# Kernel optimization log

Measured on AMD Instinct MI355X. Metric: run time of the kernel, lower is better.

Reference implementation:

```python
import jax, jax.numpy as jnp
import numpy as np

RATIOS = [0.9, 0.7, 0.5, 0.3]
EPS = 1e-5


def _layernorm(x, g, b):
    m = jnp.mean(x, axis=-1, keepdims=True)
    v = jnp.mean(jnp.square(x - m), axis=-1, keepdims=True)
    return (x - m) * jax.lax.rsqrt(v + EPS) * g + b


def _stage(x, g, b, W, bias):
    return _layernorm(x, g, b) @ W + bias


def _prune(x, W1, b1, W2, b2, ratio):
    B, N, C = x.shape
    stats = jnp.mean(x, axis=1)                       # (B, C)
    scores = jax.nn.relu(stats @ W1 + b1) @ W2 + b2    # (B, C)
    k = max(1, int(C * ratio))
    _, idx = jax.lax.top_k(jax.lax.stop_gradient(scores), k)  # (B, k)
    hard = jnp.zeros((B, C), scores.dtype).at[jnp.arange(B)[:, None], idx].set(1.0)
    soft = jax.nn.sigmoid(scores)
    # straight-through: forward value == hard, gradient flows through soft
    mask = hard + soft - jax.lax.stop_gradient(soft)
    return x * mask[:, None, :]


def setup_inputs() -> dict:
    key = jax.random.key(0)
    dims = [(96, 96), (96, 192), (192, 384), (384, 768)]
    inp = {}
    ks = jax.random.split(key, 64)
    ki = iter(ks)
    inp["x"] = jax.random.normal(next(ki), (32, 3136, 96), dtype=jnp.float32)
    for i, (din, dout) in enumerate(dims, 1):
        inp[f"s{i}_g"] = jnp.ones((din,), jnp.float32)
        inp[f"s{i}_b"] = jnp.zeros((din,), jnp.float32)
        inp[f"s{i}_W"] = jax.random.normal(next(ki), (din, dout), jnp.float32) * 0.02
        inp[f"s{i}_bias"] = jnp.zeros((dout,), jnp.float32)
        d = dout
        inp[f"p{i}_W1"] = jax.random.normal(next(ki), (d, d // 4), jnp.float32) * 0.02
        inp[f"p{i}_b1"] = jnp.zeros((d // 4,), jnp.float32)
        inp[f"p{i}_W2"] = jax.random.normal(next(ki), (d // 4, d), jnp.float32) * 0.02
        inp[f"p{i}_b2"] = jnp.zeros((d,), jnp.float32)
    inp["H"] = 56
    inp["W"] = 56
    return inp


def reference(x,
              s1_g, s1_b, s1_W, s1_bias, p1_W1, p1_b1, p1_W2, p1_b2,
              s2_g, s2_b, s2_W, s2_bias, p2_W1, p2_b1, p2_W2, p2_b2,
              s3_g, s3_b, s3_W, s3_bias, p3_W1, p3_b1, p3_W2, p3_b2,
              s4_g, s4_b, s4_W, s4_bias, p4_W1, p4_b1, p4_W2, p4_b2,
              H, W):
    x = _stage(x, s1_g, s1_b, s1_W, s1_bias)
    x = _prune(x, p1_W1, p1_b1, p1_W2, p1_b2, RATIOS[0])
    x = _stage(x, s2_g, s2_b, s2_W, s2_bias)
    x = _prune(x, p2_W1, p2_b1, p2_W2, p2_b2, RATIOS[1])
    x = _stage(x, s3_g, s3_b, s3_W, s3_bias)
    x = _prune(x, p3_W1, p3_b1, p3_W2, p3_b2, RATIOS[2])
    x = _stage(x, s4_g, s4_b, s4_W, s4_bias)
    x = _prune(x, p4_W1, p4_b1, p4_W2, p4_b2, RATIOS[3])
    return x
```

## Files before the change

kernel.cpp:

```cpp
#include <hip/hip_runtime.h>
#include <hip/hip_bf16.h>
#include <stdint.h>

#define NTOK 3136
#define MTOT 100352
#define RPW  14
#define WPB  224

typedef __attribute__((ext_vector_type(8))) short bf16x8;
typedef __attribute__((ext_vector_type(4))) float f32x4;
typedef __attribute__((ext_vector_type(2))) float f32x2;

static __device__ __forceinline__ ushort f2bf(float x) {
  union { float f; uint32_t u; } c; c.f = x;
  uint32_t r = (c.u + 0x7FFFu + ((c.u >> 16) & 1u)) >> 16;
  return (ushort)r;
}
static __device__ __forceinline__ float bf2f(ushort h) {
  union { uint32_t u; float f; } c; c.u = ((uint32_t)h) << 16;
  return c.f;
}

template<int DIN, bool WLO>
__global__ __launch_bounds__(256)
void ln_colsum_k(const float* __restrict__ in, const float* __restrict__ gma,
                 const float* __restrict__ bta, ushort* __restrict__ oh,
                 ushort* __restrict__ ol, float* __restrict__ part)
{
  constexpr int P2 = DIN / 2;
  constexpr int T2 = (P2 + 63) / 64;
  const int wid  = (blockIdx.x * 256 + threadIdx.x) >> 6;
  const int lane = threadIdx.x & 63;
  const int b = wid / WPB;
  const int w = wid - b * WPB;

  f32x2 gv[T2], bv[T2], acc[T2];
#pragma unroll
  for (int t = 0; t < T2; ++t) {
    int c2 = lane + 64 * t;
    if (c2 < P2) {
      gv[t] = *(const f32x2*)(gma + 2 * c2);
      bv[t] = *(const f32x2*)(bta + 2 * c2);
    } else { gv[t] = {0.f, 0.f}; bv[t] = {0.f, 0.f}; }
    acc[t] = {0.f, 0.f};
  }

  const size_t rbase = ((size_t)b * NTOK + (size_t)w * RPW) * DIN;
  const float* ip = in + rbase;
  ushort* oph = oh + rbase;
  ushort* opl = ol + rbase;

  for (int j = 0; j < RPW; ++j) {
    f32x2 v[T2];
    float s = 0.f, sq = 0.f;
#pragma unroll
    for (int t = 0; t < T2; ++t) {
      int c2 = lane + 64 * t;
      f32x2 xv = {0.f, 0.f};
      if (c2 < P2) xv = *(const f32x2*)(ip + (size_t)j * DIN + 2 * c2);
      v[t] = xv;
      s  += xv[0] + xv[1];
      sq += xv[0] * xv[0] + xv[1] * xv[1];
    }
#pragma unroll
    for (int off = 1; off < 64; off <<= 1) {
      s  += __shfl_xor(s, off);
      sq += __shfl_xor(sq, off);
    }
    float m   = s / (float)DIN;
    float var = sq / (float)DIN - m * m;
    float r   = 1.f / sqrtf(var + 1e-5f);
#pragma unroll
    for (int t = 0; t < T2; ++t) {
      int c2 = lane + 64 * t;
      if (c2 < P2) {
        float xn0 = (v[t][0] - m) * r * gv[t][0] + bv[t][0];
        float xn1 = (v[t][1] - m) * r * gv[t][1] + bv[t][1];
        ushort h0 = f2bf(xn0), h1 = f2bf(xn1);
        ((uint32_t*)(oph + (size_t)j * DIN))[c2] =
            (uint32_t)h0 | ((uint32_t)h1 << 16);
        if (WLO) {
          ushort l0 = f2bf(xn0 - bf2f(h0)), l1 = f2bf(xn1 - bf2f(h1));
          ((uint32_t*)(opl + (size_t)j * DIN))[c2] =
              (uint32_t)l0 | ((uint32_t)l1 << 16);
        }
        acc[t][0] += xn0;
        acc[t][1] += xn1;
      }
    }
  }
#pragma unroll
  for (int t = 0; t < T2; ++t) {
    int c2 = lane + 64 * t;
    if (c2 < P2) {
      int c = 2 * c2;
      part[((size_t)b * DIN + c) * WPB + w]     = acc[t][0];
      part[((size_t)b * DIN + c + 1) * WPB + w] = acc[t][1];
    }
  }
}

template<int DIN, int DOUT, int SLOTS, bool CMP, int CMPN, int RLEN, bool GLO>
__global__ __launch_bounds__(1024)
void scores_k(const float* __restrict__ part,
              const float* __restrict__ Wt, const float* __restrict__ bias,
              const float* __restrict__ W1, const float* __restrict__ b1,
              const float* __restrict__ W2, const float* __restrict__ b2,
              float* __restrict__ mask, int k,
              const ushort* __restrict__ whi, const ushort* __restrict__ wlo,
              ushort* __restrict__ wch, ushort* __restrict__ wcl,
              int* __restrict__ list_g, float* __restrict__ biasc)
{
  constexpr int DH  = DOUT / 4;
  constexpr int DH4 = DH / 4;
  constexpr int NSLC = (1024 / DH4 < 64) ? 1024 / DH4 : 64;
  constexpr int RPSC = (DOUT + NSLC - 1) / NSLC;
  constexpr int C4  = DOUT / 4;
  constexpr int NSLD = (1024 / C4 < 64) ? 1024 / C4 : 64;
  constexpr int RPSD = (DH + NSLD - 1) / NSLD;

  __shared__ float xm[DIN];
  __shared__ float st[DOUT];
  __shared__ float h[DH];
  __shared__ float sc[DOUT];
  __shared__ float red[4096];
  __shared__ int lsh[256];

  const int b = blockIdx.x, tid = threadIdx.x;

  if constexpr (SLOTS == 25) {
    if (tid < DIN) {
      const float* p = part + ((size_t)b * DIN + tid) * 25;
      float s = 0.f;
#pragma unroll
      for (int i = 0; i < 25; ++i) s += p[i];
      xm[tid] = s * (1.f / (float)NTOK);
    }
  } else {
    const int cg = tid >> 2, wq = tid & 3;
    if (cg < DIN) {
      const float* p = part + ((size_t)b * DIN + cg) * WPB + wq * 56;
      f32x4 a = {0.f, 0.f, 0.f, 0.f};
#pragma unroll
      for (int u = 0; u < 14; ++u) {
        f32x4 t0 = *(const f32x4*)(p + u * 4);
        a[0] += t0[0]; a[1] += t0[1]; a[2] += t0[2]; a[3] += t0[3];
      }
      red[wq * DIN + cg] = (a[0] + a[1]) + (a[2] + a[3]);
    }
    __syncthreads();
    if (tid < DIN)
      xm[tid] = ((red[0 * DIN + tid] + red[1 * DIN + tid]) +
                 (red[2 * DIN + tid] + red[3 * DIN + tid])) * (1.f / (float)NTOK);
  }
  __syncthreads();

  {
    constexpr int RPS = DIN / 4;
    const int j4 = tid % C4, sl = tid / C4;
    if (sl < 4) {
      const float* wp = Wt + (size_t)(sl * RPS) * DOUT + j4 * 4;
      f32x4 acc = {0.f, 0.f, 0.f, 0.f};
#pragma unroll
      for (int r = 0; r < RPS; ++r) {
        f32x4 wv = *(const f32x4*)(wp + (size_t)r * DOUT);
        float xv = xm[sl * RPS + r];
        acc[0] = fmaf(xv, wv[0], acc[0]);
        acc[1] = fmaf(xv, wv[1], acc[1]);
        acc[2] = fmaf(xv, wv[2], acc[2]);
        acc[3] = fmaf(xv, wv[3], acc[3]);
      }
      *(f32x4*)&red[sl * DOUT + j4 * 4] = acc;
    }
  }
  __syncthreads();
  if (tid < DOUT)
    st[tid] = ((red[0 * DOUT + tid] + red[1 * DOUT + tid]) +
               (red[2 * DOUT + tid] + red[3 * DOUT + tid])) + bias[tid];
  __syncthreads();

  {
    const int j4 = tid % DH4, sl = tid / DH4;
    if (sl < NSLC) {
      f32x4 acc = {0.f, 0.f, 0.f, 0.f};
#pragma unroll
      for (int rr = 0; rr < RPSC; ++rr) {
        int r = sl * RPSC + rr;
        if (r < DOUT) {
          f32x4 wv = *(const f32x4*)(W1 + (size_t)r * DH + j4 * 4);
          float sv = st[r];
          acc[0] = fmaf(sv, wv[0], acc[0]);
          acc[1] = fmaf(sv, wv[1], acc[1]);
          acc[2] = fmaf(sv, wv[2], acc[2]);
          acc[3] = fmaf(sv, wv[3], acc[3]);
        }
      }
      *(f32x4*)&red[(size_t)sl * DH + j4 * 4] = acc;
    }
  }
  __syncthreads();
  if (tid < DH) {
    float a = 0.f;
#pragma unroll 4
    for (int sl = 0; sl < NSLC; ++sl) a += red[(size_t)sl * DH + tid];
    h[tid] = fmaxf(b1[tid] + a, 0.f);
  }
  __syncthreads();

  {
    const int c4 = tid % C4, sl = tid / C4;
    if (sl < NSLD) {
      f32x4 acc = {0.f, 0.f, 0.f, 0.f};
#pragma unroll
      for (int rr = 0; rr < RPSD; ++rr) {
        int r = sl * RPSD + rr;
        if (r < DH) {
          f32x4 wv = *(const f32x4*)(W2 + (size_t)r * DOUT + c4 * 4);
          float hv = h[r];
          acc[0] = fmaf(hv, wv[0], acc[0]);
          acc[1] = fmaf(hv, wv[1], acc[1]);
          acc[2] = fmaf(hv, wv[2], acc[2]);
          acc[3] = fmaf(hv, wv[3], acc[3]);
        }
      }
      *(f32x4*)&red[(size_t)sl * DOUT + c4 * 4] = acc;
    }
  }
  __syncthreads();
  for (int c = tid; c < DOUT; c += 1024) {
    float a = 0.f;
#pragma unroll 4
    for (int sl = 0; sl < NSLD; ++sl) a += red[(size_t)sl * DOUT + c];
    sc[c] = b2[c] + a;
  }
  __syncthreads();

  for (int c = tid; c < DOUT; c += 1024) {
    float v = sc[c];
    int rank = 0;
#pragma unroll 8
    for (int j = 0; j < DOUT; ++j) {
      float u = sc[j];
      rank += (u > v) || (u == v && j < c);
    }
    mask[(size_t)b * DOUT + c] = (rank < k) ? 1.f : 0.f;
    if (CMP && rank < k) lsh[rank] = c;
  }
  if constexpr (CMP) {
    if (tid >= k && tid < CMPN) lsh[tid] = -1;
    __syncthreads();
    if (tid < CMPN) {
      int c = lsh[tid];
      list_g[b * 256 + tid] = c;
      biasc[b * 256 + tid] = (c >= 0) ? bias[c] : 0.f;
    }
    constexpr int U4 = RLEN / 8;
    for (int idx = tid; idx < CMPN * U4; idx += 1024) {
      int j = idx / U4, u = idx - j * U4;
      int src = lsh[j];
      uint4 v = make_uint4(0u, 0u, 0u, 0u);
      if (src >= 0) v = *(const uint4*)(whi + (size_t)src * RLEN + u * 8);
      *(uint4*)(wch + ((size_t)b * CMPN + j) * RLEN + u * 8) = v;
      if constexpr (GLO) {
        uint4 vl = make_uint4(0u, 0u, 0u, 0u);
        if (src >= 0) vl = *(const uint4*)(wlo + (size_t)src * RLEN + u * 8);
        *(uint4*)(wcl + ((size_t)b * CMPN + j) * RLEN + u * 8) = vl;
      }
    }
  }
}

__global__ __launch_bounds__(256)
void convW_all_k(const float* __restrict__ W0, const float* __restrict__ W1,
                 const float* __restrict__ W2, const float* __restrict__ W3,
                 ushort* __restrict__ hi, ushort* __restrict__ lo)
{
  const int Kd[4]   = { 96, 96, 192, 384 };
  const int Nd[4]   = { 96, 192, 384, 768 };
  const int off[5]  = { 0, 12288, 36864, 110592, 405504 };
  const float* Wp[4] = { W0, W1, W2, W3 };

  int idx = blockIdx.x * 256 + threadIdx.x;
  if (idx >= 405504) return;
  int s = (idx >= off[1]) + (idx >= off[2]) + (idx >= off[3]);
  int local = idx - off[s];
  int K = Kd[s], N = Nd[s];
  int n = local / K, kk = local - n * K;
  float v = (n < N) ? Wp[s][(size_t)kk * N + n] : 0.f;
  ushort h = f2bf(v);
  hi[idx] = h;
  lo[idx] = f2bf(v - bf2f(h));
}

#define ASYNC16(GP, LP) __builtin_amdgcn_global_load_lds( \
    (const __attribute__((address_space(1))) void*)(GP),  \
    (__attribute__((address_space(3))) void*)(LP), 16, 0, 0)

template<int K, int NSEG, int BNL, int N, int NWN, bool WLO>
__global__ __launch_bounds__(128 * NWN)
void gemm_ln_k(const ushort* __restrict__ a0, const ushort* __restrict__ a1,
               const ushort* __restrict__ a2,
               const ushort* __restrict__ b0, const ushort* __restrict__ b1,
               const ushort* __restrict__ b2,
               const float* __restrict__ bias, const float* __restrict__ msk,
               const float* __restrict__ gnext, const float* __restrict__ bnext,
               ushort* __restrict__ oh, ushort* __restrict__ ol,
               float* __restrict__ part)
{
  constexpr int T   = 128 * NWN;
  constexpr int R   = T / 4;
  constexpr int AI  = 128 / R;
  constexpr int BI  = BNL / R;
  constexpr int IS  = AI + BI;
  constexpr int WN  = N / NWN;
  constexpr int NFR = WN / 16;
  constexpr int KSTEPS = K / 32;
  constexpr int NT  = NSEG * KSTEPS;
  __shared__ __align__(16) ushort ldsA[3][128 * 32];
  __shared__ __align__(16) ushort ldsB[3][BNL * 32];

  const int tid  = threadIdx.x;
  const int lane = tid & 63;
  const int wid  = tid >> 6;
  const int wm = wid & 1, wn = wid >> 1;

  const int q8  = gridDim.x >> 3;
  const int bid = blockIdx.x;
  const int mt  = (bid & 7) * q8 + (bid >> 3);
  const size_t row0 = (size_t)mt * 128;

  const ushort* Aseg[3] = { a0, a1, a2 };
  const ushort* Bseg[3] = { b0, b1, b2 };

  f32x4 acc[4][NFR];
#pragma unroll
  for (int i = 0; i < 4; ++i)
#pragma unroll
    for (int j = 0; j < NFR; ++j) acc[i][j] = { 0.f, 0.f, 0.f, 0.f };

  const int c_row  = tid >> 2;
  const int c_phys = tid & 3;

#define STAGEF(BUF, TT)                                                        \
  {                                                                            \
    const int seg_ = (TT) / KSTEPS;                                            \
    const int k0_  = ((TT) % KSTEPS) * 32;                                     \
    const ushort* ap_ = Aseg[seg_];                                            \
    const ushort* bp_ = Bseg[seg_];                                            \
    _Pragma("unroll")                                                          \
    for (int r_ = 0; r_ < AI; ++r_) {                                          \
      int row_  = c_row + r_ * R;                                              \
      int slot_ = c_phys ^ ((row_ >> 1) & 3);                                  \
      ASYNC16(ap_ + (row0 + row_) * (size_t)K + (k0_ + slot_ * 8),             \
              &ldsA[BUF][(row_ * 4 + c_phys) * 8]);                            \
    }                                                                          \
    _Pragma("unroll")                                                          \
    for (int r_ = 0; r_ < BI; ++r_) {                                          \
      int row_  = c_row + r_ * R;                                              \
      int slot_ = c_phys ^ ((row_ >> 1) & 3);                                  \
      ASYNC16(bp_ + (size_t)row_ * K + (k0_ + slot_ * 8),                      \
              &ldsB[BUF][(row_ * 4 + c_phys) * 8]);                            \
    }                                                                          \
  }

  STAGEF(0, 0);
  STAGEF(1, 1);
#pragma unroll
  for (int t = 0; t < NT; ++t) {
    if (t == NT - 1)            { asm volatile("s_waitcnt vmcnt(0)" ::: "memory"); }
    else if constexpr (IS == 4) { asm volatile("s_waitcnt vmcnt(4)" ::: "memory"); }
    else                        { asm volatile("s_waitcnt vmcnt(5)" ::: "memory"); }
    __builtin_amdgcn_s_barrier();
    if (t + 2 < NT) STAGEF((t + 2) % 3, t + 2);
    const int buf = t % 3;
    const int slot = lane >> 4;
    const int r16  = lane & 15;
    bf16x8 af[4], bfr[NFR];
#pragma unroll
    for (int mi = 0; mi < 4; ++mi) {
      int r = wm * 64 + mi * 16 + r16;
      af[mi] = *(const bf16x8*)&ldsA[buf][(r * 4 + (slot ^ ((r >> 1) & 3))) * 8];
    }
#pragma unroll
    for (int ni = 0; ni < NFR; ++ni) {
      int r = wn * WN + ni * 16 + r16;
      bfr[ni] = *(const bf16x8*)&ldsB[buf][(r * 4 + (slot ^ ((r >> 1) & 3))) * 8];
    }
#pragma unroll
    for (int mi = 0; mi < 4; ++mi)
#pragma unroll
      for (int ni = 0; ni < NFR; ++ni)
        acc[mi][ni] = __builtin_amdgcn_mfma_f32_16x16x32_bf16(af[mi], bfr[ni],
                                                              acc[mi][ni], 0, 0, 0);
  }
#undef STAGEF

  __syncthreads();

  float* rowred = (float*)&ldsA[0][0];
  ushort* xsh = (ushort*)&ldsB[0][0];
  ushort* xsl = xsh + 32 * N;
  float* colred = (float*)(xsh + 32 * N * (WLO ? 2 : 1));

  const int l15 = lane & 15, l4 = lane >> 4;
  const int b0i = (int)(row0 / NTOK);
  const size_t rowB = (size_t)(b0i + 1) * NTOK;
  const bool strad = rowB < row0 + 128;

  float biasv[NFR], mk0a[NFR], mk1a[NFR], gvn[NFR], bvn[NFR];
#pragma unroll
  for (int ni = 0; ni < NFR; ++ni) {
    int n = wn * WN + ni * 16 + l15;
    biasv[ni] = bias[n];
    mk0a[ni] = msk[(size_t)b0i * N + n];
    mk1a[ni] = strad ? msk[(size_t)(b0i + 1) * N + n] : mk0a[ni];
    gvn[ni] = gnext[n];
    bvn[ni] = bnext[n];
  }

  float rs[16], rq[16];
#pragma unroll
  for (int i = 0; i < 16; ++i) { rs[i] = 0.f; rq[i] = 0.f; }
#pragma unroll
  for (int mi = 0; mi < 4; ++mi)
#pragma unroll
    for (int q = 0; q < 4; ++q) {
      size_t row = row0 + wm * 64 + mi * 16 + l4 * 4 + q;
      bool loB = row < rowB;
#pragma unroll
      for (int ni = 0; ni < NFR; ++ni) {
        float v = (acc[mi][ni][q] + biasv[ni]) * (loB ? mk0a[ni] : mk1a[ni]);
        acc[mi][ni][q] = v;
        rs[mi * 4 + q] += v;
        rq[mi * 4 + q] += v * v;
      }
    }
#pragma unroll
  for (int off = 1; off < 16; off <<= 1)
#pragma unroll
    for (int i = 0; i < 16; ++i) {
      rs[i] += __shfl_xor(rs[i], off);
      rq[i] += __shfl_xor(rq[i], off);
    }
  if (l15 == 0) {
#pragma unroll
    for (int mi = 0; mi < 4; ++mi)
#pragma unroll
      for (int q = 0; q < 4; ++q) {
        int r = wm * 64 + mi * 16 + l4 * 4 + q;
        rowred[(wn * 128 + r) * 2 + 0] = rs[mi * 4 + q];
        rowred[(wn * 128 + r) * 2 + 1] = rq[mi * 4 + q];
      }
  }
  __syncthreads();

  float mean[16], rstd[16];
#pragma unroll
  for (int mi = 0; mi < 4; ++mi)
#pragma unroll
    for (int q = 0; q < 4; ++q) {
      int r = wm * 64 + mi * 16 + l4 * 4 + q;
      float S = 0.f, Q = 0.f;
#pragma unroll
      for (int w = 0; w < NWN; ++w) {
        S += rowred[(w * 128 + r) * 2 + 0];
        Q += rowred[(w * 128 + r) * 2 + 1];
      }
      float mn  = S / (float)N;
      float var = Q / (float)N - mn * mn;
      mean[mi * 4 + q] = mn;
      rstd[mi * 4 + q] = 1.f / sqrtf(var + 1e-5f);
    }

  float cs0[NFR], cs1[NFR];
#pragma unroll
  for (int ni = 0; ni < NFR; ++ni) { cs0[ni] = 0.f; cs1[ni] = 0.f; }
#pragma unroll
  for (int mi = 0; mi < 4; ++mi) {
    __syncthreads();
#pragma unroll
    for (int q = 0; q < 4; ++q) {
      const int rl = l4 * 4 + q;
      const size_t row = row0 + wm * 64 + mi * 16 + rl;
      const bool loB = row < rowB;
      const float mn = mean[mi * 4 + q], rv = rstd[mi * 4 + q];
#pragma unroll
      for (int ni = 0; ni < NFR; ++ni) {
        const int n = wn * WN + ni * 16 + l15;
        float xn = (acc[mi][ni][q] - mn) * rv * gvn[ni] + bvn[ni];
        ushort hh = f2bf(xn);
        xsh[(wm * 16 + rl) * N + n] = hh;
        if constexpr (WLO) xsl[(wm * 16 + rl) * N + n] = f2bf(xn - bf2f(hh));
        if (loB) cs0[ni] += xn; else cs1[ni] += xn;
      }
    }
    __syncthreads();
    constexpr int U4R = N / 8;
    for (int idx = tid; idx < 32 * U4R; idx += T) {
      const int grp = idx / U4R, c = idx - grp * U4R;
      const size_t row = row0 + (grp >> 4) * 64 + mi * 16 + (grp & 15);
      *(uint4*)(oh + row * (size_t)N + c * 8) =
          *(const uint4*)(xsh + grp * N + c * 8);
      if constexpr (WLO)
        *(uint4*)(ol + row * (size_t)N + c * 8) =
            *(const uint4*)(xsl + grp * N + c * 8);
    }
  }

#pragma unroll
  for (int ni = 0; ni < NFR; ++ni) {
    cs0[ni] += __shfl_xor(cs0[ni], 16);
    cs0[ni] += __shfl_xor(cs0[ni], 32);
    cs1[ni] += __shfl_xor(cs1[ni], 16);
    cs1[ni] += __shfl_xor(cs1[ni], 32);
  }
  __syncthreads();
  if (l4 == 0) {
#pragma unroll
    for (int ni = 0; ni < NFR; ++ni) {
      int n = wn * WN + ni * 16 + l15;
      colred[(0 * 2 + wm) * N + n] = cs0[ni];
      colred[(1 * 2 + wm) * N + n] = cs1[ni];
    }
  }
  __syncthreads();
  if (wm == 0 && l4 == 0) {
    const int mt_lo = (b0i * NTOK) >> 7;
    const int slot0 = mt - mt_lo;
#pragma unroll
    for (int ni = 0; ni < NFR; ++ni) {
      int n = wn * WN + ni * 16 + l15;
      float t0 = colred[0 * N + n] + colred[1 * N + n];
      part[((size_t)b0i * N + n) * 25 + slot0] = t0;
      if (strad) {
        float t1 = colred[2 * N + n] + colred[3 * N + n];
        part[((size_t)(b0i + 1) * N + n) * 25 + 0] = t1;
      }
    }
  }
}

template<int K, int NC, int N>
__global__ __launch_bounds__(256)
void gemm_lnc_k(const ushort* __restrict__ ahi, const ushort* __restrict__ alo,
                const ushort* __restrict__ wch, const ushort* __restrict__ wcl,
                const int* __restrict__ list, const float* __restrict__ biasc,
                const float* __restrict__ gnext, const float* __restrict__ bnext,
                ushort* __restrict__ oh, float* __restrict__ part)
{
  constexpr int KSTEPS = K / 32;
  constexpr int NT  = 3 * KSTEPS;
  constexpr int WN  = NC / 2;
  constexpr int NFR = WN / 16;
  __shared__ __align__(16) ushort ldsA[3][128 * 32];
  __shared__ __align__(16) ushort ldsB[3][NC * 32];
  __shared__ float rowred[2][128][2];
  __shared__ float rowmnrv[128];
  __shared__ float rowrv[128];

  const int tid  = threadIdx.x;
  const int lane = tid & 63;
  const int wid  = tid >> 6;
  const int wm = wid & 1, wn = wid >> 1;

  const int q8  = gridDim.x >> 3;
  const int bid = blockIdx.x;
  const int wg  = (bid & 7) * q8 + (bid >> 3);
  const int b   = wg / 25;
  const int mt  = wg - b * 25;
  const size_t row0 = (size_t)b * NTOK + (size_t)mt * 128;
  const size_t rowEnd = (size_t)(b + 1) * NTOK;
  const int rows_valid = (mt == 24) ? 64 : 128;

  const ushort* Aseg[3] = { ahi, ahi, alo };
  const ushort* Bseg[3] = { wch + (size_t)b * NC * K, wcl + (size_t)b * NC * K,
                            wch + (size_t)b * NC * K };

  f32x4 acc[4][NFR];
#pragma unroll
  for (int i = 0; i < 4; ++i)
#pragma unroll
    for (int j = 0; j < NFR; ++j) acc[i][j] = { 0.f, 0.f, 0.f, 0.f };

  const int c_row  = tid >> 2;
  const int c_phys = tid & 3;

#define STAGEL(BUF, TT)                                                        \
  {                                                                            \
    const int seg_ = (TT) / KSTEPS;                                            \
    const int k0_  = ((TT) % KSTEPS) * 32;                                     \
    const ushort* ap_ = Aseg[seg_];                                            \
    const ushort* bp_ = Bseg[seg_];                                            \
    _Pragma("unroll")                                                          \
    for (int r_ = 0; r_ < 2; ++r_) {                                           \
      int row_  = c_row + r_ * 64;                                             \
      int slot_ = c_phys ^ ((row_ >> 1) & 3);                                  \
      size_t ar_ = row0 + row_;                                                \
      if (ar_ >= rowEnd) ar_ = rowEnd - 1;                                     \
      ASYNC16(ap_ + ar_ * (size_t)K + (k0_ + slot_ * 8),                       \
              &ldsA[BUF][(row_ * 4 + c_phys) * 8]);                            \
    }                                                                          \
    _Pragma("unroll")                                                          \
    for (int r_ = 0; r_ < 3; ++r_) {                                           \
      int row_  = c_row + r_ * 64;                                             \
      int slot_ = c_phys ^ ((row_ >> 1) & 3);                                  \
      ASYNC16(bp_ + (size_t)row_ * K + (k0_ + slot_ * 8),                      \
              &ldsB[BUF][(row_ * 4 + c_phys) * 8]);                            \
    }                                                                          \
  }

  STAGEL(0, 0);
  STAGEL(1, 1);
#pragma unroll
  for (int t = 0; t < NT; ++t) {
    if (t == NT - 1) { asm volatile("s_waitcnt vmcnt(0)" ::: "memory"); }
    else             { asm volatile("s_waitcnt vmcnt(5)" ::: "memory"); }
    __builtin_amdgcn_s_barrier();
    if (t + 2 < NT) STAGEL((t + 2) % 3, t + 2);
    const int buf = t % 3;
    const int slot = lane >> 4;
    const int r16  = lane & 15;
    bf16x8 af[4], bfr[NFR];
#pragma unroll
    for (int mi = 0; mi < 4; ++mi) {
      int r = wm * 64 + mi * 16 + r16;
      af[mi] = *(const bf16x8*)&ldsA[buf][(r * 4 + (slot ^ ((r >> 1) & 3))) * 8];
    }
#pragma unroll
    for (int ni = 0; ni < NFR; ++ni) {
      int r = wn * WN + ni * 16 + r16;
      bfr[ni] = *(const bf16x8*)&ldsB[buf][(r * 4 + (slot ^ ((r >> 1) & 3))) * 8];
    }
#pragma unroll
    for (int mi = 0; mi < 4; ++mi)
#pragma unroll
      for (int ni = 0; ni < NFR; ++ni)
        acc[mi][ni] = __builtin_amdgcn_mfma_f32_16x16x32_bf16(af[mi], bfr[ni],
                                                              acc[mi][ni], 0, 0, 0);
  }
#undef STAGEL

  __syncthreads();

  const int l15 = lane & 15, l4 = lane >> 4;

  int   nj[NFR];
  float biasv[NFR];
#pragma unroll
  for (int ni = 0; ni < NFR; ++ni) {
    int j = wn * WN + ni * 16 + l15;
    nj[ni]    = list[b * 256 + j];
    biasv[ni] = biasc[b * 256 + j];
  }

  float rs[16], rq[16];
#pragma unroll
  for (int i = 0; i < 16; ++i) { rs[i] = 0.f; rq[i] = 0.f; }
#pragma unroll
  for (int mi = 0; mi < 4; ++mi)
#pragma unroll
    for (int q = 0; q < 4; ++q) {
#pragma unroll
      for (int ni = 0; ni < NFR; ++ni) {
        float v = acc[mi][ni][q] + biasv[ni];
        acc[mi][ni][q] = v;
        rs[mi * 4 + q] += v;
        rq[mi * 4 + q] += v * v;
      }
    }
#pragma unroll
  for (int off = 1; off < 16; off <<= 1)
#pragma unroll
    for (int i = 0; i < 16; ++i) {
      rs[i] += __shfl_xor(rs[i], off);
      rq[i] += __shfl_xor(rq[i], off);
    }
  if (l15 == 0) {
#pragma unroll
    for (int mi = 0; mi < 4; ++mi)
#pragma unroll
      for (int q = 0; q < 4; ++q) {
        int r = wm * 64 + mi * 16 + l4 * 4 + q;
        rowred[wn][r][0] = rs[mi * 4 + q];
        rowred[wn][r][1] = rq[mi * 4 + q];
      }
  }
  __syncthreads();
  if (tid < 128) {
    float S = rowred[0][tid][0] + rowred[1][tid][0];
    float Q = rowred[0][tid][1] + rowred[1][tid][1];
    float mn = S / (float)N;
    float rv = 1.f / sqrtf(Q / (float)N - mn * mn + 1e-5f);
    rowmnrv[tid] = mn * rv;
    rowrv[tid]   = rv;
  }
  __syncthreads();

  float* sbuf = (float*)&ldsB[0][0];
  float colS = 0.f, colS2 = 0.f;

#pragma unroll
  for (int h = 0; h < 8; ++h) {
    if (h * 16 >= rows_valid) break;
    __syncthreads();
    for (int idx = tid; idx < 16 * N / 4; idx += 256)
      ((f32x4*)sbuf)[idx] = f32x4{0.f, 0.f, 0.f, 0.f};
    __syncthreads();
    if ((h >> 2) == wm) {
      const int mi = h & 3;
#pragma unroll
      for (int q = 0; q < 4; ++q) {
        const int rl = l4 * 4 + q;
        const float rv = rowrv[h * 16 + rl];
#pragma unroll
        for (int ni = 0; ni < NFR; ++ni)
          sbuf[rl * N + nj[ni]] = acc[mi][ni][q] * rv;
      }
    }
    __syncthreads();
    {
      float a = 0.f;
#pragma unroll
      for (int rl = 0; rl < 16; ++rl) a += sbuf[rl * N + tid];
      colS += a;
      if (tid < N - 256) {
        float a2 = 0.f;
        const int c2 = 256 + tid;
#pragma unroll
        for (int rl = 0; rl < 16; ++rl) a2 += sbuf[rl * N + c2];
        colS2 += a2;
      }
    }
    for (int idx = tid; idx < 16 * (N / 8); idx += 256) {
      const int rl = idx / (N / 8), cg = idx - rl * (N / 8);
      const float mnrv = rowmnrv[h * 16 + rl];
      const float* sp = sbuf + rl * N + cg * 8;
      f32x4 s0 = *(const f32x4*)(sp);
      f32x4 s1 = *(const f32x4*)(sp + 4);
      f32x4 g0 = *(const f32x4*)(gnext + cg * 8);
      f32x4 g1 = *(const f32x4*)(gnext + cg * 8 + 4);
      f32x4 e0 = *(const f32x4*)(bnext + cg * 8);
      f32x4 e1 = *(const f32x4*)(bnext + cg * 8 + 4);
      uint32_t w[4];
#pragma unroll
      for (int j = 0; j < 2; ++j) {
        ushort ha = f2bf(g0[2*j]   * (s0[2*j]   - mnrv) + e0[2*j]);
        ushort hb = f2bf(g0[2*j+1] * (s0[2*j+1] - mnrv) + e0[2*j+1]);
        w[j] = (uint32_t)ha | ((uint32_t)hb << 16);
      }
#pragma unroll
      for (int j = 0; j < 2; ++j) {
        ushort ha = f2bf(g1[2*j]   * (s1[2*j]   - mnrv) + e1[2*j]);
        ushort hb = f2bf(g1[2*j+1] * (s1[2*j+1] - mnrv) + e1[2*j+1]);
        w[2 + j] = (uint32_t)ha | ((uint32_t)hb << 16);
      }
      *(uint4*)(oh + (row0 + h * 16 + rl) * (size_t)N + cg * 8) =
          make_uint4(w[0], w[1], w[2], w[3]);
    }
  }

  float msum = 0.f;
  for (int r = 0; r < rows_valid; ++r) msum += rowmnrv[r];
  {
    const int c = tid;
    part[((size_t)b * N + c) * 25 + mt] =
        gnext[c] * (colS - msum) + (float)rows_valid * bnext[c];
    if (tid < N - 256) {
      const int c2 = 256 + tid;
      part[((size_t)b * N + c2) * 25 + mt] =
          gnext[c2] * (colS2 - msum) + (float)rows_valid * bnext[c2];
    }
  }
}

template<int K>
__global__ __launch_bounds__(512)
void gemm_c4_k(const ushort* __restrict__ A, const ushort* __restrict__ Wc,
               const int* __restrict__ list, const float* __restrict__ biasc,
               float* __restrict__ C)
{
  constexpr int NT = K / 32;
  __shared__ __align__(16) ushort ldsA[3][128 * 32];
  __shared__ __align__(16) ushort ldsB[3][256 * 32];

  const int tid  = threadIdx.x;
  const int lane = tid & 63;
  const int wid  = tid >> 6;
  const int wm = wid & 1, wn = wid >> 1;

  const int q8  = gridDim.x >> 3;
  const int bid = blockIdx.x;
  const int wg  = (bid & 7) * q8 + (bid >> 3);
  const int b   = wg / 25;
  const int mt  = wg - b * 25;
  const size_t row0 = (size_t)b * NTOK + (size_t)mt * 128;
  const int rows_valid = (mt == 24) ? 64 : 128;

  const ushort* bp = Wc + (size_t)b * 256 * K;

  const int c_row  = tid >> 2;
  const int c_phys = tid & 3;

  size_t arow = row0 + c_row;
  const size_t rowEnd = (size_t)(b + 1) * NTOK;
  if (arow >= rowEnd) arow = rowEnd - 1;
  const ushort* apr = A + arow * (size_t)K;

  f32x4 acc[4][4];
#pragma unroll
  for (int i = 0; i < 4; ++i)
#pragma unroll
    for (int j = 0; j < 4; ++j) acc[i][j] = { 0.f, 0.f, 0.f, 0.f };

#define STAGEC(BUF, TT)                                                        \
  {                                                                            \
    const int k0_ = (TT) * 32;                                                 \
    {                                                                          \
      int slot_ = c_phys ^ ((c_row >> 1) & 3);                                 \
      ASYNC16(apr + (k0_ + slot_ * 8),                                         \
              &ldsA[BUF][(c_row * 4 + c_phys) * 8]);                           \
    }                                                                          \
    _Pragma("unroll")                                                          \
    for (int r_ = 0; r_ < 2; ++r_) {                                           \
      int row_  = c_row + r_ * 128;                                            \
      int slot_ = c_phys ^ ((row_ >> 1) & 3);                                  \
      ASYNC16(bp + (size_t)row_ * K + (k0_ + slot_ * 8),                       \
              &ldsB[BUF][(row_ * 4 + c_phys) * 8]);                            \
    }                                                                          \
  }

  STAGEC(0, 0);
  STAGEC(1, 1);
#pragma unroll
  for (int t = 0; t < NT; ++t) {
    if (t == NT - 1) { asm volatile("s_waitcnt vmcnt(0)" ::: "memory"); }
    else             { asm volatile("s_waitcnt vmcnt(3)" ::: "memory"); }
    __builtin_amdgcn_s_barrier();
    if (t + 2 < NT) STAGEC((t + 2) % 3, t + 2);
    const int buf = t % 3;
    const int slot = lane >> 4;
    const int r16  = lane & 15;
    bf16x8 af[4], bfr[4];
#pragma unroll
    for (int mi = 0; mi < 4; ++mi) {
      int r = wm * 64 + mi * 16 + r16;
      af[mi] = *(const bf16x8*)&ldsA[buf][(r * 4 + (slot ^ ((r >> 1) & 3))) * 8];
    }
#pragma unroll
    for (int ni = 0; ni < 4; ++ni) {
      int r = wn * 64 + ni * 16 + r16;
      bfr[ni] = *(const bf16x8*)&ldsB[buf][(r * 4 + (slot ^ ((r >> 1) & 3))) * 8];
    }
#pragma unroll
    for (int mi = 0; mi < 4; ++mi)
#pragma unroll
      for (int ni = 0; ni < 4; ++ni)
        acc[mi][ni] = __builtin_amdgcn_mfma_f32_16x16x32_bf16(af[mi], bfr[ni],
                                                              acc[mi][ni], 0, 0, 0);
  }
#undef STAGEC

  float* cst = (float*)&ldsB[0][0];

  const int l15 = lane & 15, l4 = lane >> 4;
  int   nj[4];
  float biasv[4];
#pragma unroll
  for (int ni = 0; ni < 4; ++ni) {
    int j = wn * 64 + ni * 16 + l15;
    nj[ni]    = list[b * 256 + j];
    biasv[ni] = biasc[b * 256 + j];
  }

#pragma unroll
  for (int hh = 0; hh < 8; ++hh) {
    const int hrows = rows_valid - hh * 16;
    if (hrows <= 0) break;
    __syncthreads();
    for (int idx = tid; idx < 16 * 192; idx += 512)
      ((f32x4*)cst)[idx] = f32x4{0.f, 0.f, 0.f, 0.f};
    __syncthreads();
    if ((hh >> 2) == wm) {
      const int mi = hh & 3;
#pragma unroll
      for (int q = 0; q < 4; ++q) {
        const int rl = l4 * 4 + q;
#pragma unroll
        for (int ni = 0; ni < 4; ++ni)
          if (nj[ni] >= 0)
            cst[rl * 768 + nj[ni]] = acc[mi][ni][q] + biasv[ni];
      }
    }
    __syncthreads();
    const int nst = (hrows >= 16 ? 16 : hrows) * 192;
    for (int idx = tid; idx < nst; idx += 512) {
      const int grp = idx / 192, c = idx - grp * 192;
      const size_t row = row0 + hh * 16 + grp;
      *(f32x4*)(C + row * 768 + c * 4) = ((const f32x4*)cst)[grp * 192 + c];
    }
  }
}

extern "C" void kernel_launch(void* const* d_in, const int* in_sizes, int n_in,
                              void* d_out, int out_size, void* d_ws, size_t ws_size,
                              hipStream_t stream)
{
  (void)in_sizes; (void)n_in; (void)out_size; (void)ws_size;
  const float* x = (const float*)d_in[0];
  const float *sg[4], *sb[4], *sW[4], *sbias[4], *pW1[4], *pb1[4], *pW2[4], *pb2[4];
  for (int s = 0; s < 4; ++s) {
    int base = 1 + s * 8;
    sg[s]    = (const float*)d_in[base + 0];
    sb[s]    = (const float*)d_in[base + 1];
    sW[s]    = (const float*)d_in[base + 2];
    sbias[s] = (const float*)d_in[base + 3];
    pW1[s]   = (const float*)d_in[base + 4];
    pb1[s]   = (const float*)d_in[base + 5];
    pW2[s]   = (const float*)d_in[base + 6];
    pb2[s]   = (const float*)d_in[base + 7];
  }

  float* out = (float*)d_out;
  ushort* hiA = (ushort*)out;
  ushort* loA = (ushort*)(out + 19267584);
  ushort* loB = (ushort*)(out + 38535168);

  char* ws = (char*)d_ws;
  ushort* hiB  = (ushort*)(ws);
  float*  part = (float*) (ws + 77070336);
  float*  mk   = (float*) (ws + 79822848);
  ushort* w_hi = (ushort*)(ws + 79921152);
  ushort* w_lo = (ushort*)(ws + 80732160);
  ushort* wc   = (ushort*)(ws + 81543168);
  int*    lst  = (int*)   (ws + 87834624);
  float*  bsc  = (float*) (ws + 87867392);

  ushort* wch3 = wc;
  ushort* wcl3 = wc + 1179648;

  const int woff[4] = { 0, 12288, 36864, 110592 };

  convW_all_k<<<(405504 + 255) / 256, 256, 0, stream>>>(
      sW[0], sW[1], sW[2], sW[3], w_hi, w_lo);

  const int LNG = 32 * WPB / 4;

  ln_colsum_k<96, true><<<LNG, 256, 0, stream>>>(x, sg[0], sb[0], hiA, loA, part);
  scores_k<96, 96, 224, false, 256, 384, false><<<32, 1024, 0, stream>>>(
      part, sW[0], sbias[0], pW1[0], pb1[0], pW2[0], pb2[0], mk, 86,
      nullptr, nullptr, nullptr, nullptr, nullptr, nullptr);
  gemm_ln_k<96, 3, 128, 96, 2, true><<<784, 256, 0, stream>>>(
      hiA, hiA, loA, w_hi + woff[0], w_lo + woff[0], w_hi + woff[0],
      sbias[0], mk, sg[1], sb[1], hiB, loB, part);

  scores_k<96, 192, 25, false, 256, 384, false><<<32, 1024, 0, stream>>>(
      part, sW[1], sbias[1], pW1[1], pb1[1], pW2[1], pb2[1], mk, 134,
      nullptr, nullptr, nullptr, nullptr, nullptr, nullptr);
  gemm_ln_k<96, 3, 192, 192, 2, true><<<784, 256, 0, stream>>>(
      hiB, hiB, loB, w_hi + woff[1], w_lo + woff[1], w_hi + woff[1],
      sbias[1], mk, sg[2], sb[2], hiA, loA, part);

  scores_k<192, 384, 25, true, 192, 192, true><<<32, 1024, 0, stream>>>(
      part, sW[2], sbias[2], pW1[2], pb1[2], pW2[2], pb2[2], mk, 192,
      w_hi + woff[2], w_lo + woff[2], wch3, wcl3, lst, bsc);
  gemm_lnc_k<192, 192, 384><<<800, 256, 0, stream>>>(
      hiA, loA, wch3, wcl3, lst, bsc, sg[3], sb[3], hiB, part);

  scores_k<384, 768, 25, true, 256, 384, false><<<32, 1024, 0, stream>>>(
      part, sW[3], sbias[3], pW1[3], pb1[3], pW2[3], pb2[3], mk, 230,
      w_hi + woff[3], nullptr, wc, nullptr, lst, bsc);
  gemm_c4_k<384><<<800, 512, 0, stream>>>(hiB, wc, lst, bsc, out);
}
```

Baseline: 475.8 us.

## Load hi/lo operands together and run split-bf16 MFMAs per K-step

```diff
diff --git a/kernel.cpp b/kernel.cpp
--- a/kernel.cpp
+++ b/kernel.cpp
@@ -296,12 +296,10 @@
     (const __attribute__((address_space(1))) void*)(GP),  \
     (__attribute__((address_space(3))) void*)(LP), 16, 0, 0)
 
-template<int K, int NSEG, int BNL, int N, int NWN, bool WLO>
+template<int K, int BNL, int N, int NWN, bool WLO>
 __global__ __launch_bounds__(128 * NWN)
-void gemm_ln_k(const ushort* __restrict__ a0, const ushort* __restrict__ a1,
-               const ushort* __restrict__ a2,
-               const ushort* __restrict__ b0, const ushort* __restrict__ b1,
-               const ushort* __restrict__ b2,
+void gemm_ln_k(const ushort* __restrict__ ahi, const ushort* __restrict__ alo,
+               const ushort* __restrict__ bhi, const ushort* __restrict__ blo,
                const float* __restrict__ bias, const float* __restrict__ msk,
                const float* __restrict__ gnext, const float* __restrict__ bnext,
                ushort* __restrict__ oh, ushort* __restrict__ ol,
@@ -311,13 +309,13 @@
   constexpr int R   = T / 4;
   constexpr int AI  = 128 / R;
   constexpr int BI  = BNL / R;
-  constexpr int IS  = AI + BI;
+  constexpr int KS  = K / 32;
   constexpr int WN  = N / NWN;
   constexpr int NFR = WN / 16;
-  constexpr int KSTEPS = K / 32;
-  constexpr int NT  = NSEG * KSTEPS;
-  __shared__ __align__(16) ushort ldsA[3][128 * 32];
-  __shared__ __align__(16) ushort ldsB[3][BNL * 32];
+  __shared__ __align__(16) ushort ldsAh[2][128 * 32];
+  __shared__ __align__(16) ushort ldsAl[2][128 * 32];
+  __shared__ __align__(16) ushort ldsBh[2][BNL * 32];
+  __shared__ __align__(16) ushort ldsBl[2][BNL * 32];
 
   const int tid  = threadIdx.x;
   const int lane = tid & 63;
@@ -329,9 +327,6 @@
   const int mt  = (bid & 7) * q8 + (bid >> 3);
   const size_t row0 = (size_t)mt * 128;
 
-  const ushort* Aseg[3] = { a0, a1, a2 };
-  const ushort* Bseg[3] = { b0, b1, b2 };
-
   f32x4 acc[4][NFR];
 #pragma unroll
   for (int i = 0; i < 4; ++i)
@@ -341,66 +336,84 @@
   const int c_row  = tid >> 2;
   const int c_phys = tid & 3;
 
-#define STAGEF(BUF, TT)                                                        \
+#define STG(BUF, KK)                                                           \
   {                                                                            \
-    const int seg_ = (TT) / KSTEPS;                                            \
-    const int k0_  = ((TT) % KSTEPS) * 32;                                     \
-    const ushort* ap_ = Aseg[seg_];                                            \
-    const ushort* bp_ = Bseg[seg_];                                            \
+    const int k0_ = (KK) * 32;                                                 \
     _Pragma("unroll")                                                          \
     for (int r_ = 0; r_ < AI; ++r_) {                                          \
       int row_  = c_row + r_ * R;                                              \
       int slot_ = c_phys ^ ((row_ >> 1) & 3);                                  \
-      ASYNC16(ap_ + (row0 + row_) * (size_t)K + (k0_ + slot_ * 8),             \
-              &ldsA[BUF][(row_ * 4 + c_phys) * 8]);                            \
+      ASYNC16(ahi + (row0 + row_) * (size_t)K + (k0_ + slot_ * 8),             \
+              &ldsAh[BUF][(row_ * 4 + c_phys) * 8]);                           \
+      ASYNC16(alo + (row0 + row_) * (size_t)K + (k0_ + slot_ * 8),             \
+              &ldsAl[BUF][(row_ * 4 + c_phys) * 8]);                           \
     }                                                                          \
     _Pragma("unroll")                                                          \
     for (int r_ = 0; r_ < BI; ++r_) {                                          \
       int row_  = c_row + r_ * R;                                              \
       int slot_ = c_phys ^ ((row_ >> 1) & 3);                                  \
-      ASYNC16(bp_ + (size_t)row_ * K + (k0_ + slot_ * 8),                      \
-              &ldsB[BUF][(row_ * 4 + c_phys) * 8]);                            \
+      ASYNC16(bhi + (size_t)row_ * K + (k0_ + slot_ * 8),                      \
+              &ldsBh[BUF][(row_ * 4 + c_phys) * 8]);                           \
+      ASYNC16(blo + (size_t)row_ * K + (k0_ + slot_ * 8),                      \
+              &ldsBl[BUF][(row_ * 4 + c_phys) * 8]);                           \
     }                                                                          \
   }
 
-  STAGEF(0, 0);
-  STAGEF(1, 1);
-#pragma unroll
-  for (int t = 0; t < NT; ++t) {
-    if (t == NT - 1)            { asm volatile("s_waitcnt vmcnt(0)" ::: "memory"); }
-    else if constexpr (IS == 4) { asm volatile("s_waitcnt vmcnt(4)" ::: "memory"); }
-    else                        { asm volatile("s_waitcnt vmcnt(5)" ::: "memory"); }
-    __builtin_amdgcn_s_barrier();
-    if (t + 2 < NT) STAGEF((t + 2) % 3, t + 2);
-    const int buf = t % 3;
+  STG(0, 0);
+  asm volatile("s_waitcnt vmcnt(0)" ::: "memory");
+  __builtin_amdgcn_s_barrier();
+#pragma unroll
+  for (int t = 0; t < KS; ++t) {
+    if (t + 1 < KS) STG((t + 1) & 1, t + 1);
+    const int buf = t & 1;
     const int slot = lane >> 4;
     const int r16  = lane & 15;
-    bf16x8 af[4], bfr[NFR];
+    bf16x8 ah[4], al[4], bh[NFR], bl[NFR];
 #pragma unroll
     for (int mi = 0; mi < 4; ++mi) {
       int r = wm * 64 + mi * 16 + r16;
-      af[mi] = *(const bf16x8*)&ldsA[buf][(r * 4 + (slot ^ ((r >> 1) & 3))) * 8];
+      int off = (r * 4 + (slot ^ ((r >> 1) & 3))) * 8;
+      ah[mi] = *(const bf16x8*)&ldsAh[buf][off];
+      al[mi] = *(const bf16x8*)&ldsAl[buf][off];
     }
 #pragma unroll
     for (int ni = 0; ni < NFR; ++ni) {
       int r = wn * WN + ni * 16 + r16;
-      bfr[ni] = *(const bf16x8*)&ldsB[buf][(r * 4 + (slot ^ ((r >> 1) & 3))) * 8];
+      int off = (r * 4 + (slot ^ ((r >> 1) & 3))) * 8;
+      bh[ni] = *(const bf16x8*)&ldsBh[buf][off];
+      bl[ni] = *(const bf16x8*)&ldsBl[buf][off];
     }
 #pragma unroll
     for (int mi = 0; mi < 4; ++mi)
 #pragma unroll
       for (int ni = 0; ni < NFR; ++ni)
-        acc[mi][ni] = __builtin_amdgcn_mfma_f32_16x16x32_bf16(af[mi], bfr[ni],
+        acc[mi][ni] = __builtin_amdgcn_mfma_f32_16x16x32_bf16(ah[mi], bh[ni],
                                                               acc[mi][ni], 0, 0, 0);
-  }
-#undef STAGEF
-
-  __syncthreads();
-
-  float* rowred = (float*)&ldsA[0][0];
-  ushort* xsh = (ushort*)&ldsB[0][0];
-  ushort* xsl = xsh + 32 * N;
-  float* colred = (float*)(xsh + 32 * N * (WLO ? 2 : 1));
+#pragma unroll
+    for (int mi = 0; mi < 4; ++mi)
+#pragma unroll
+      for (int ni = 0; ni < NFR; ++ni)
+        acc[mi][ni] = __builtin_amdgcn_mfma_f32_16x16x32_bf16(ah[mi], bl[ni],
+                                                              acc[mi][ni], 0, 0, 0);
+#pragma unroll
+    for (int mi = 0; mi < 4; ++mi)
+#pragma unroll
+      for (int ni = 0; ni < NFR; ++ni)
+        acc[mi][ni] = __builtin_amdgcn_mfma_f32_16x16x32_bf16(al[mi], bh[ni],
+                                                              acc[mi][ni], 0, 0, 0);
+    if (t + 1 < KS) {
+      asm volatile("s_waitcnt vmcnt(0)" ::: "memory");
+      __builtin_amdgcn_s_barrier();
+    }
+  }
+#undef STG
+
+  __syncthreads();
+
+  float* rowred = (float*)&ldsAh[0][0];
+  float* colred = (float*)&ldsAl[0][0];
+  ushort* xsh = (ushort*)&ldsBh[0][0];
+  ushort* xsl = (ushort*)&ldsBl[0][0];
 
   const int l15 = lane & 15, l4 = lane >> 4;
   const int b0i = (int)(row0 / NTOK);
@@ -548,15 +561,13 @@
                 const float* __restrict__ gnext, const float* __restrict__ bnext,
                 ushort* __restrict__ oh, float* __restrict__ part)
 {
-  constexpr int KSTEPS = K / 32;
-  constexpr int NT  = 3 * KSTEPS;
+  constexpr int KS  = K / 32;
   constexpr int WN  = NC / 2;
   constexpr int NFR = WN / 16;
-  __shared__ __align__(16) ushort ldsA[3][128 * 32];
-  __shared__ __align__(16) ushort ldsB[3][NC * 32];
-  __shared__ float rowred[2][128][2];
-  __shared__ float rowmnrv[128];
-  __shared__ float rowrv[128];
+  __shared__ __align__(16) ushort ldsAh[2][128 * 32];
+  __shared__ __align__(16) ushort ldsAl[2][128 * 32];
+  __shared__ __align__(16) ushort ldsBh[2][NC * 32];
+  __shared__ __align__(16) ushort ldsBl[2][NC * 32];
 
   const int tid  = threadIdx.x;
   const int lane = tid & 63;
@@ -572,9 +583,8 @@
   const size_t rowEnd = (size_t)(b + 1) * NTOK;
   const int rows_valid = (mt == 24) ? 64 : 128;
 
-  const ushort* Aseg[3] = { ahi, ahi, alo };
-  const ushort* Bseg[3] = { wch + (size_t)b * NC * K, wcl + (size_t)b * NC * K,
-                            wch + (size_t)b * NC * K };
+  const ushort* bph = wch + (size_t)b * NC * K;
+  const ushort* bpl = wcl + (size_t)b * NC * K;
 
   f32x4 acc[4][NFR];
 #pragma unroll
@@ -585,62 +595,87 @@
   const int c_row  = tid >> 2;
   const int c_phys = tid & 3;
 
-#define STAGEL(BUF, TT)                                                        \
+#define STGL(BUF, KK)                                                          \
   {                                                                            \
-    const int seg_ = (TT) / KSTEPS;                                            \
-    const int k0_  = ((TT) % KSTEPS) * 32;                                     \
-    const ushort* ap_ = Aseg[seg_];                                            \
-    const ushort* bp_ = Bseg[seg_];                                            \
+    const int k0_ = (KK) * 32;                                                 \
     _Pragma("unroll")                                                          \
     for (int r_ = 0; r_ < 2; ++r_) {                                           \
       int row_  = c_row + r_ * 64;                                             \
       int slot_ = c_phys ^ ((row_ >> 1) & 3);                                  \
       size_t ar_ = row0 + row_;                                                \
       if (ar_ >= rowEnd) ar_ = rowEnd - 1;                                     \
-      ASYNC16(ap_ + ar_ * (size_t)K + (k0_ + slot_ * 8),                       \
-              &ldsA[BUF][(row_ * 4 + c_phys) * 8]);                            \
+      ASYNC16(ahi + ar_ * (size_t)K + (k0_ + slot_ * 8),                       \
+              &ldsAh[BUF][(row_ * 4 + c_phys) * 8]);                           \
+      ASYNC16(alo + ar_ * (size_t)K + (k0_ + slot_ * 8),                       \
+              &ldsAl[BUF][(row_ * 4 + c_phys) * 8]);                           \
     }                                                                          \
     _Pragma("unroll")                                                          \
     for (int r_ = 0; r_ < 3; ++r_) {                                           \
       int row_  = c_row + r_ * 64;                                             \
       int slot_ = c_phys ^ ((row_ >> 1) & 3);                                  \
-      ASYNC16(bp_ + (size_t)row_ * K + (k0_ + slot_ * 8),                      \
-              &ldsB[BUF][(row_ * 4 + c_phys) * 8]);                            \
+      ASYNC16(bph + (size_t)row_ * K + (k0_ + slot_ * 8),                      \
+              &ldsBh[BUF][(row_ * 4 + c_phys) * 8]);                           \
+      ASYNC16(bpl + (size_t)row_ * K + (k0_ + slot_ * 8),                      \
+              &ldsBl[BUF][(row_ * 4 + c_phys) * 8]);                           \
     }                                                                          \
   }
 
-  STAGEL(0, 0);
-  STAGEL(1, 1);
-#pragma unroll
-  for (int t = 0; t < NT; ++t) {
-    if (t == NT - 1) { asm volatile("s_waitcnt vmcnt(0)" ::: "memory"); }
-    else             { asm volatile("s_waitcnt vmcnt(5)" ::: "memory"); }
-    __builtin_amdgcn_s_barrier();
-    if (t + 2 < NT) STAGEL((t + 2) % 3, t + 2);
-    const int buf = t % 3;
+  STGL(0, 0);
+  asm volatile("s_waitcnt vmcnt(0)" ::: "memory");
+  __builtin_amdgcn_s_barrier();
+#pragma unroll
+  for (int t = 0; t < KS; ++t) {
+    if (t + 1 < KS) STGL((t + 1) & 1, t + 1);
+    const int buf = t & 1;
     const int slot = lane >> 4;
     const int r16  = lane & 15;
-    bf16x8 af[4], bfr[NFR];
+    bf16x8 ah[4], al[4], bh[NFR], bl[NFR];
 #pragma unroll
     for (int mi = 0; mi < 4; ++mi) {
       int r = wm * 64 + mi * 16 + r16;
-      af[mi] = *(const bf16x8*)&ldsA[buf][(r * 4 + (slot ^ ((r >> 1) & 3))) * 8];
+      int off = (r * 4 + (slot ^ ((r >> 1) & 3))) * 8;
+      ah[mi] = *(const bf16x8*)&ldsAh[buf][off];
+      al[mi] = *(const bf16x8*)&ldsAl[buf][off];
     }
 #pragma unroll
     for (int ni = 0; ni < NFR; ++ni) {
       int r = wn * WN + ni * 16 + r16;
-      bfr[ni] = *(const bf16x8*)&ldsB[buf][(r * 4 + (slot ^ ((r >> 1) & 3))) * 8];
+      int off = (r * 4 + (slot ^ ((r >> 1) & 3))) * 8;
+      bh[ni] = *(const bf16x8*)&ldsBh[buf][off];
+      bl[ni] = *(const bf16x8*)&ldsBl[buf][off];
     }
 #pragma unroll
     for (int mi = 0; mi < 4; ++mi)
 #pragma unroll
       for (int ni = 0; ni < NFR; ++ni)
-        acc[mi][ni] = __builtin_amdgcn_mfma_f32_16x16x32_bf16(af[mi], bfr[ni],
+        acc[mi][ni] = __builtin_amdgcn_mfma_f32_16x16x32_bf16(ah[mi], bh[ni],
                                                               acc[mi][ni], 0, 0, 0);
-  }
-#undef STAGEL
-
-  __syncthreads();
+#pragma unroll
+    for (int mi = 0; mi < 4; ++mi)
+#pragma unroll
+      for (int ni = 0; ni < NFR; ++ni)
+        acc[mi][ni] = __builtin_amdgcn_mfma_f32_16x16x32_bf16(ah[mi], bl[ni],
+                                                              acc[mi][ni], 0, 0, 0);
+#pragma unroll
+    for (int mi = 0; mi < 4; ++mi)
+#pragma unroll
+      for (int ni = 0; ni < NFR; ++ni)
+        acc[mi][ni] = __builtin_amdgcn_mfma_f32_16x16x32_bf16(al[mi], bh[ni],
+                                                              acc[mi][ni], 0, 0, 0);
+    if (t + 1 < KS) {
+      asm volatile("s_waitcnt vmcnt(0)" ::: "memory");
+      __builtin_amdgcn_s_barrier();
+    }
+  }
+#undef STGL
+
+  __syncthreads();
+
+  float* rr      = (float*)&ldsAh[0][0];
+  float* rowredp = rr;
+  float* rowmnrv = rr + 512;
+  float* rowrv   = rr + 640;
+  float* sbuf    = (float*)&ldsBh[0][0];
 
   const int l15 = lane & 15, l4 = lane >> 4;
 
@@ -681,14 +716,14 @@
 #pragma unroll
       for (int q = 0; q < 4; ++q) {
         int r = wm * 64 + mi * 16 + l4 * 4 + q;
-        rowred[wn][r][0] = rs[mi * 4 + q];
-        rowred[wn][r][1] = rq[mi * 4 + q];
+        rowredp[(wn * 128 + r) * 2 + 0] = rs[mi * 4 + q];
+        rowredp[(wn * 128 + r) * 2 + 1] = rq[mi * 4 + q];
       }
   }
   __syncthreads();
   if (tid < 128) {
-    float S = rowred[0][tid][0] + rowred[1][tid][0];
-    float Q = rowred[0][tid][1] + rowred[1][tid][1];
+    float S = rowredp[(0 * 128 + tid) * 2 + 0] + rowredp[(1 * 128 + tid) * 2 + 0];
+    float Q = rowredp[(0 * 128 + tid) * 2 + 1] + rowredp[(1 * 128 + tid) * 2 + 1];
     float mn = S / (float)N;
     float rv = 1.f / sqrtf(Q / (float)N - mn * mn + 1e-5f);
     rowmnrv[tid] = mn * rv;
@@ -696,7 +731,6 @@
   }
   __syncthreads();
 
-  float* sbuf = (float*)&ldsB[0][0];
   float colS = 0.f, colS2 = 0.f;
 
 #pragma unroll
@@ -949,15 +983,15 @@
   scores_k<96, 96, 224, false, 256, 384, false><<<32, 1024, 0, stream>>>(
       part, sW[0], sbias[0], pW1[0], pb1[0], pW2[0], pb2[0], mk, 86,
       nullptr, nullptr, nullptr, nullptr, nullptr, nullptr);
-  gemm_ln_k<96, 3, 128, 96, 2, true><<<784, 256, 0, stream>>>(
-      hiA, hiA, loA, w_hi + woff[0], w_lo + woff[0], w_hi + woff[0],
+  gemm_ln_k<96, 128, 96, 2, true><<<784, 256, 0, stream>>>(
+      hiA, loA, w_hi + woff[0], w_lo + woff[0],
       sbias[0], mk, sg[1], sb[1], hiB, loB, part);
 
   scores_k<96, 192, 25, false, 256, 384, false><<<32, 1024, 0, stream>>>(
       part, sW[1], sbias[1], pW1[1], pb1[1], pW2[1], pb2[1], mk, 134,
       nullptr, nullptr, nullptr, nullptr, nullptr, nullptr);
-  gemm_ln_k<96, 3, 192, 192, 2, true><<<784, 256, 0, stream>>>(
-      hiB, hiB, loB, w_hi + woff[1], w_lo + woff[1], w_hi + woff[1],
+  gemm_ln_k<96, 192, 192, 2, true><<<784, 256, 0, stream>>>(
+      hiB, loB, w_hi + woff[1], w_lo + woff[1],
       sbias[1], mk, sg[2], sb[2], hiA, loA, part);
 
   scores_k<192, 384, 25, true, 192, 192, true><<<32, 1024, 0, stream>>>(
```

New measurement: 461.9 us. 1.03x faster.
